# Performance work log

Measured on AMD Instinct MI355X. Metric: run time of the kernel, lower is better.

The kernel has to match this reference:

```python
import jax, jax.numpy as jnp
import numpy as np


def setup_inputs() -> dict:
    key = jax.random.key(0)
    ks = jax.random.split(key, 8)
    C, mid, H, W, N = 256, 32, 64, 64, 4
    x = jax.random.normal(ks[0], (N, C, H, W), dtype=jnp.float32)
    # 1x1 conv weights squeezed to [out_ch, in_ch]; small init scale like kaiming
    s = 1.0 / np.sqrt(C)
    Wq = jax.random.normal(ks[1], (mid, C), dtype=jnp.float32) * s
    bq = jnp.zeros((mid,), dtype=jnp.float32)
    Wk = jax.random.normal(ks[2], (mid, C), dtype=jnp.float32) * s
    bk = jnp.zeros((mid,), dtype=jnp.float32)
    Wv = jax.random.normal(ks[3], (C, C), dtype=jnp.float32) * s
    bv = jnp.zeros((C,), dtype=jnp.float32)
    gamma = jax.random.uniform(ks[4], (1,), dtype=jnp.float32)
    return {"x": x, "Wq": Wq, "bq": bq, "Wk": Wk, "bk": bk, "Wv": Wv, "bv": bv, "gamma": gamma}


def reference(x, Wq, bq, Wk, bk, Wv, bv, gamma):
    N, C, H, W = x.shape
    xf = x.reshape(N, C, H * W)  # [N, C, S]
    # 1x1 convs are channel-mixing GEMMs
    Q = jnp.einsum('mc,ncs->nms', Wq, xf) + bq[:, None]  # [N, mid, S]
    K = jnp.einsum('mc,ncs->nms', Wk, xf) + bk[:, None]  # [N, mid, S]
    V = jnp.einsum('dc,ncs->nds', Wv, xf) + bv[:, None]  # [N, C, S]
    # A[s, t] = softmax_t( Q[:, s] . K[:, t] )
    scores = jnp.einsum('nms,nmt->nst', Q, K)            # [N, S, S]
    A = jax.nn.softmax(scores, axis=-1)
    # out = V @ A^T : out[:, s] = sum_t A[s, t] * V[:, t]
    out = jnp.einsum('ndt,nst->nds', V, A).reshape(N, C, H, W)
    return x + gamma[0] * out
```

## Files before the change

### kernel.cpp

```cpp
#include <hip/hip_runtime.h>
#include <hip/hip_bf16.h>
#include <stdint.h>

#define S_LEN 4096
#define LOG2E 1.44269504088896f
#define SMAX  40.0f

typedef __attribute__((ext_vector_type(8)))  short short8;
typedef __attribute__((ext_vector_type(8)))  _Float16 half8;
typedef __attribute__((ext_vector_type(4)))  float f32x4;
typedef __attribute__((ext_vector_type(16))) float f32x16;
typedef __attribute__((ext_vector_type(2)))  unsigned int u32x2;
typedef __attribute__((ext_vector_type(4)))  unsigned int u32x4;

#define OFF_V     ((size_t)0)
#define OFF_QT    (OFF_V + (size_t)(8u<<20))
#define OFF_KT    (OFF_QT + (size_t)(1u<<20))
#define OFF_WVBF  (OFF_KT + (size_t)(1u<<20))
#define OFF_WQH   (OFF_WVBF + (size_t)(128*1024))
#define OFF_WQL   (OFF_WQH + (size_t)(16*1024))
#define OFF_WKH   (OFF_WQL + (size_t)(16*1024))
#define OFF_WKL   (OFF_WKH + (size_t)(16*1024))

__device__ __forceinline__ unsigned short f2bf(float f) {
    __hip_bfloat16 h = __float2bfloat16(f);
    return *(unsigned short*)&h;
}
__device__ __forceinline__ float bf2f(unsigned short u) {
    return __bfloat162float(*(__hip_bfloat16*)&u);
}
__device__ __forceinline__ unsigned pk2(float a, float b) {
    return (unsigned)f2bf(a) | ((unsigned)f2bf(b) << 16);
}
__device__ __forceinline__ unsigned short f2h(float f) {
    _Float16 h = (_Float16)f;
    return *(unsigned short*)&h;
}
union S8U { u32x4 u; short8 s; };
union H8U { short8 s; half8 h; };

__device__ __forceinline__ void gl_lds16(const void* g, void* l) {
    __builtin_amdgcn_global_load_lds(
        (const __attribute__((address_space(1))) unsigned int*)g,
        (__attribute__((address_space(3))) unsigned int*)(unsigned int)(size_t)l,
        16, 0, 0);
}

#define Z16 {0.f,0.f,0.f,0.f,0.f,0.f,0.f,0.f,0.f,0.f,0.f,0.f,0.f,0.f,0.f,0.f}
#define MFMA32  __builtin_amdgcn_mfma_f32_32x32x16_bf16
#define MFMA32H __builtin_amdgcn_mfma_f32_32x32x16_f16

__global__ __launch_bounds__(256) void wprep(const float* __restrict__ Wq,
                                             const float* __restrict__ Wk,
                                             const float* __restrict__ Wv,
                                             unsigned short* __restrict__ wvbf,
                                             unsigned short* __restrict__ wqh,
                                             unsigned short* __restrict__ wql,
                                             unsigned short* __restrict__ wkh,
                                             unsigned short* __restrict__ wkl)
{
    const int b = blockIdx.x;
    if (b < 64) {
        int i = b * 1024 + threadIdx.x * 4;
        f32x4 w = *(const f32x4*)(Wv + i);
        u32x2 pk;
        pk[0] = pk2(w[0], w[1]);
        pk[1] = pk2(w[2], w[3]);
        *(u32x2*)(wvbf + i) = pk;
    } else {
        const float* Wsrc = (b == 64) ? Wq : Wk;
        float scale = (b == 64) ? LOG2E : 1.f;
        unsigned short* oh = (b == 64) ? wqh : wkh;
        unsigned short* ol = (b == 64) ? wql : wkl;
        int t = threadIdx.x;
#pragma unroll
        for (int ii = 0; ii < 4; ii++) {
            int ent = t * 4 + ii;
            int m = ent & 31, hh = (ent >> 5) & 1, kc = ent >> 6;
#pragma unroll
            for (int e = 0; e < 8; e++) {
                int c = kc * 16 + hh * 8 + e;
                float wv = Wsrc[m * 256 + c] * scale;
                unsigned short wh = f2bf(wv);
                oh[ent * 8 + e] = wh;
                ol[ent * 8 + e] = f2bf(wv - bf2f(wh));
            }
        }
    }
}

__global__ __launch_bounds__(256) void qkv_fused(
    const float* __restrict__ x,
    const unsigned short* __restrict__ wqh, const unsigned short* __restrict__ wql,
    const unsigned short* __restrict__ wkh, const unsigned short* __restrict__ wkl,
    const unsigned short* __restrict__ wvbf,
    const float* __restrict__ bq, const float* __restrict__ bk, const float* __restrict__ bv,
    unsigned short* __restrict__ qt, unsigned short* __restrict__ kt,
    unsigned char* __restrict__ Vsw)
{
    const int tid = threadIdx.x;
    const int bidx = blockIdx.x;
    const int n = bidx >> 7, t0 = (bidx & 127) * 32;
    const int w = tid >> 6, l = tid & 63;
    const int l31 = l & 31, h = l >> 5;

    __shared__ float xs[256 * 36];

    {
        const int c0 = tid >> 3;
        const int tq = (tid & 7) * 4;
        const float* xp = x + ((size_t)n * 256 + c0) * S_LEN + t0 + tq;
#pragma unroll
        for (int p = 0; p < 8; p++) {
            f32x4 v = *(const f32x4*)(xp + (size_t)p * 32 * S_LEN);
            *(f32x4*)(&xs[(c0 + p * 32) * 36 + tq]) = v;
        }
    }
    __syncthreads();

    if (w < 2) {
        const unsigned short* WH = w ? wkh : wqh;
        const unsigned short* WL = w ? wkl : wql;
        f32x16 a = Z16;
#pragma unroll
        for (int kc = 0; kc < 16; kc++) {
            short8 ah, al;
#pragma unroll
            for (int e = 0; e < 8; e++) {
                float f = xs[(kc * 16 + h * 8 + e) * 36 + l31];
                unsigned short hb = f2bf(f);
                ah[e] = (short)hb;
                al[e] = (short)f2bf(f - bf2f(hb));
            }
            const short8 bh = *(const short8*)(WH + ((kc * 2 + h) * 32 + l31) * 8);
            const short8 bl = *(const short8*)(WL + ((kc * 2 + h) * 32 + l31) * 8);
            a = MFMA32(ah, bh, a, 0, 0, 0);
            a = MFMA32(al, bh, a, 0, 0, 0);
            a = MFMA32(ah, bl, a, 0, 0, 0);
        }
        float bias = w ? bk[l31] : bq[l31] * LOG2E;
        unsigned short* oh = w ? kt : qt;
#pragma unroll
        for (int r = 0; r < 16; r++) {
            int trow = (r & 3) + 8 * (r >> 2) + 4 * h;
            size_t o = ((size_t)n * S_LEN + t0 + trow) * 32 + l31;
            oh[o] = f2h(a[r] + bias);
        }
    } else {
        const int dh = w - 2;
        f32x16 acc[4];
#pragma unroll
        for (int dt = 0; dt < 4; dt++) acc[dt] = (f32x16)Z16;
#pragma unroll
        for (int kc = 0; kc < 16; kc++) {
            short8 ah;
#pragma unroll
            for (int e = 0; e < 8; e++)
                ah[e] = (short)f2bf(xs[(kc * 16 + h * 8 + e) * 36 + l31]);
#pragma unroll
            for (int dt = 0; dt < 4; dt++) {
                const short8 b = *(const short8*)(wvbf +
                    (size_t)(dh * 128 + dt * 32 + l31) * 256 + kc * 16 + h * 8);
                acc[dt] = MFMA32(ah, b, acc[dt], 0, 0, 0);
            }
        }
        unsigned char* img = Vsw + ((size_t)(n * 128) + (t0 >> 5)) * 16384;
#pragma unroll
        for (int dt = 0; dt < 4; dt++) {
            int d = dh * 128 + dt * 32 + l31;
            float bvv = bv[d];
#pragma unroll
            for (int g = 0; g < 4; g++) {
                u32x2 pkv;
                pkv[0] = pk2(acc[dt][4*g+0] + bvv, acc[dt][4*g+1] + bvv);
                pkv[1] = pk2(acc[dt][4*g+2] + bvv, acc[dt][4*g+3] + bvv);
                *(u32x2*)(img + (g >> 1) * 8192 + d * 32 + h * 16 + (g & 1) * 8) = pkv;
            }
        }
    }
}

__global__ __launch_bounds__(512, 2) void attn(
    const unsigned short* __restrict__ qt, const unsigned short* __restrict__ kt,
    const unsigned char* __restrict__ Vsw, const float* __restrict__ x,
    const float* __restrict__ gamma, float* __restrict__ out)
{
    const int bid = blockIdx.x;
    const int n = bid & 3;
    const int S0 = (bid >> 2) * 64;
    const int tid = threadIdx.x;
    const int w = tid >> 6, l = tid & 63;
    const int i = w & 1, q = w >> 1;
    const int l31 = l & 31, h = l >> 5;

    __shared__ __align__(16) unsigned char smem[131072 + 1024];
    float* mldsp = (float*)(smem + 131072);

    const size_t qb = ((size_t)n * S_LEN + S0 + i * 32 + l31) * 32 + 8 * h;
    H8U q0, q1;
    q0.s = *(const short8*)(qt + qb);
    q1.s = *(const short8*)(qt + qb + 16);

    f32x16 acc[8];
#pragma unroll
    for (int dt = 0; dt < 8; dt++) acc[dt] = (f32x16)Z16;
    float l_run = 0.f;

    const unsigned short* Kt = kt + (size_t)n * S_LEN * 32;
    const unsigned char* Vimg = Vsw + ((size_t)n * 128 + (size_t)q * 32) * 16384 + i * 8192;
    unsigned char* bufA = smem + (q * 2) * 16384;

    {
        const unsigned char* sp = Vimg + l * 16;
#pragma unroll
        for (int k = 0; k < 8; k++)
            gl_lds16(sp + k * 1024, bufA + i * 8192 + k * 1024);
    }
    size_t kb = (size_t)(q * 1024 + l31) * 32 + 8 * h;
    H8U k0, k1;
    k0.s = *(const short8*)(Kt + kb);
    k1.s = *(const short8*)(Kt + kb + 16);
    short8 paA = {0,0,0,0,0,0,0,0}, paB = {0,0,0,0,0,0,0,0};
    __syncthreads();

    const int vread = l31 * 32 + h * 16;

    for (int j = 0; j < 32; ++j) {
        __builtin_amdgcn_s_setprio(1);
        f32x16 sD = Z16;
        sD = MFMA32H(k0.h, q0.h, sD, 0, 0, 0);
        sD = MFMA32H(k1.h, q1.h, sD, 0, 0, 0);
        __builtin_amdgcn_s_setprio(0);

        if (j < 31) {
            kb += 1024;
            k0.s = *(const short8*)(Kt + kb);
            k1.s = *(const short8*)(Kt + kb + 16);
        }

        if (j > 0) {
            const unsigned char* rb = bufA + (1 - (j & 1)) * 16384;
            __builtin_amdgcn_s_setprio(1);
#pragma unroll
            for (int dt = 0; dt < 8; dt++) {
                const unsigned char* vrow = rb + dt * 1024 + vread;
                short8 v0 = *(const short8*)(vrow);
                short8 v1 = *(const short8*)(vrow + 8192);
                acc[dt] = MFMA32(v0, paA, acc[dt], 0, 0, 0);
                acc[dt] = MFMA32(v1, paB, acc[dt], 0, 0, 0);
            }
            __builtin_amdgcn_s_setprio(0);
        }

        float pe[16];
#pragma unroll
        for (int r = 0; r < 16; r++) pe[r] = __builtin_amdgcn_exp2f(sD[r] - SMAX);
        float ls = ((pe[0] + pe[1]) + (pe[2] + pe[3])) + ((pe[4] + pe[5]) + (pe[6] + pe[7]))
                 + ((pe[8] + pe[9]) + (pe[10] + pe[11])) + ((pe[12] + pe[13]) + (pe[14] + pe[15]));
        l_run += ls;

        unsigned pb[8];
#pragma unroll
        for (int i2 = 0; i2 < 8; i2++) pb[i2] = pk2(pe[2 * i2], pe[2 * i2 + 1]);
        S8U ca, cb;
        ca.u = (u32x4){pb[0], pb[1], pb[2], pb[3]};
        cb.u = (u32x4){pb[4], pb[5], pb[6], pb[7]};
        paA = ca.s;
        paB = cb.s;

        __syncthreads();

        if (j < 31) {
            const unsigned char* sp = Vimg + (size_t)(j + 1) * 16384 + l * 16;
            unsigned char* wb = bufA + ((j + 1) & 1) * 16384;
#pragma unroll
            for (int k = 0; k < 8; k++)
                gl_lds16(sp + k * 1024, wb + i * 8192 + k * 1024);
        }
    }

    {
        const unsigned char* rb = bufA + 16384;
        __builtin_amdgcn_s_setprio(1);
#pragma unroll
        for (int dt = 0; dt < 8; dt++) {
            const unsigned char* vrow = rb + dt * 1024 + vread;
            short8 v0 = *(const short8*)(vrow);
            short8 v1 = *(const short8*)(vrow + 8192);
            acc[dt] = MFMA32(v0, paA, acc[dt], 0, 0, 0);
            acc[dt] = MFMA32(v1, paB, acc[dt], 0, 0, 0);
        }
        __builtin_amdgcn_s_setprio(0);
    }

    l_run += __shfl_xor(l_run, 32);
    if (h == 0) mldsp[(q * 2 + i) * 32 + l31] = l_run;
    __syncthreads();

    float rden = 1.f / (mldsp[(0 * 2 + i) * 32 + l31] + mldsp[(1 * 2 + i) * 32 + l31]
                      + mldsp[(2 * 2 + i) * 32 + l31] + mldsp[(3 * 2 + i) * 32 + l31]);
    const float g = gamma[0];
    const int s = S0 + i * 32 + l31;

#pragma unroll
    for (int rb2 = 0; rb2 < 2; rb2++) {
        __syncthreads();
        unsigned char* myreg = smem + q * 32768 + i * 16384;
#pragma unroll
        for (int dtl = 0; dtl < 4; dtl++) {
            int dt = rb2 * 4 + dtl;
#pragma unroll
            for (int qd = 0; qd < 4; qd++) {
                f32x4 v = { acc[dt][4*qd], acc[dt][4*qd+1],
                            acc[dt][4*qd+2], acc[dt][4*qd+3] };
                *(f32x4*)(myreg + dtl * 4096 + qd * 1024 + l * 16) = v;
            }
        }
        __syncthreads();
        const int dtc = rb2 * 4 + q;
#pragma unroll
        for (int qd = 0; qd < 4; qd++) {
            f32x4 vs = {0.f, 0.f, 0.f, 0.f};
#pragma unroll
            for (int qq = 0; qq < 4; qq++) {
                f32x4 v = *(const f32x4*)(smem + qq * 32768 + i * 16384
                                          + q * 4096 + qd * 1024 + l * 16);
                vs[0] += v[0]; vs[1] += v[1]; vs[2] += v[2]; vs[3] += v[3];
            }
#pragma unroll
            for (int j = 0; j < 4; j++) {
                int d = dtc * 32 + j + 8 * qd + 4 * h;
                size_t idx = ((size_t)n * 256 + d) * S_LEN + s;
                out[idx] = x[idx] + g * vs[j] * rden;
            }
        }
    }
}

extern "C" void kernel_launch(void* const* d_in, const int* in_sizes, int n_in,
                              void* d_out, int out_size, void* d_ws, size_t ws_size,
                              hipStream_t stream) {
    const float* x     = (const float*)d_in[0];
    const float* Wq    = (const float*)d_in[1];
    const float* bq    = (const float*)d_in[2];
    const float* Wk    = (const float*)d_in[3];
    const float* bk    = (const float*)d_in[4];
    const float* Wv    = (const float*)d_in[5];
    const float* bv    = (const float*)d_in[6];
    const float* gamma = (const float*)d_in[7];
    float* out = (float*)d_out;

    unsigned char* ws = (unsigned char*)d_ws;
    unsigned char*  Vsw  = ws + OFF_V;
    unsigned short* qt   = (unsigned short*)(ws + OFF_QT);
    unsigned short* kt   = (unsigned short*)(ws + OFF_KT);
    unsigned short* wvbf = (unsigned short*)(ws + OFF_WVBF);
    unsigned short* wqh  = (unsigned short*)(ws + OFF_WQH);
    unsigned short* wql  = (unsigned short*)(ws + OFF_WQL);
    unsigned short* wkh  = (unsigned short*)(ws + OFF_WKH);
    unsigned short* wkl  = (unsigned short*)(ws + OFF_WKL);

    wprep<<<dim3(66), dim3(256), 0, stream>>>(Wq, Wk, Wv, wvbf, wqh, wql, wkh, wkl);
    qkv_fused<<<dim3(512), dim3(256), 0, stream>>>(x, wqh, wql, wkh, wkl, wvbf,
                                                   bq, bk, bv, qt, kt, Vsw);
    attn<<<dim3(256), dim3(512), 0, stream>>>(qt, kt, Vsw, x, gamma, out);
}
```

Measured before the change: 82.49 us.

## Stage V projection writes through LDS and stagger exp/MFMA phases across waves

In the projection kernel, the V tile is first written into shared memory in its swizzled layout, then copied to global memory with coalesced 16-byte stores by all threads. Matching barriers are added to the Q/K branch. In the attention loop, half the waves run the PV MFMAs before the exp/softmax work and the other half run exp first. This lets MFMA and transcendental work from different waves overlap, and the setprio around the QK MFMAs is removed. The cost is extra barriers and an LDS round trip in the projection kernel, plus some code duplication.

After: 98.97 us. +20.0%, slower.

```diff
diff --git a/kernel.cpp b/kernel.cpp
--- a/kernel.cpp
+++ b/kernel.cpp
@@ -146,6 +146,8 @@
             size_t o = ((size_t)n * S_LEN + t0 + trow) * 32 + l31;
             oh[o] = f2h(a[r] + bias);
         }
+        __syncthreads();
+        __syncthreads();
     } else {
         const int dh = w - 2;
         f32x16 acc[4];
@@ -164,7 +166,8 @@
                 acc[dt] = MFMA32(ah, b, acc[dt], 0, 0, 0);
             }
         }
-        unsigned char* img = Vsw + ((size_t)(n * 128) + (t0 >> 5)) * 16384;
+        __syncthreads();
+        unsigned char* vimg = (unsigned char*)xs;
 #pragma unroll
         for (int dt = 0; dt < 4; dt++) {
             int d = dh * 128 + dt * 32 + l31;
@@ -174,9 +177,19 @@
                 u32x2 pkv;
                 pkv[0] = pk2(acc[dt][4*g+0] + bvv, acc[dt][4*g+1] + bvv);
                 pkv[1] = pk2(acc[dt][4*g+2] + bvv, acc[dt][4*g+3] + bvv);
-                *(u32x2*)(img + (g >> 1) * 8192 + d * 32 + h * 16 + (g & 1) * 8) = pkv;
-            }
-        }
+                *(u32x2*)(vimg + (g >> 1) * 8192 + d * 32 + h * 16 + (g & 1) * 8) = pkv;
+            }
+        }
+        __syncthreads();
+    }
+
+    {
+        unsigned char* img = Vsw + ((size_t)(n * 128) + (t0 >> 5)) * 16384;
+        const unsigned char* vimg = (const unsigned char*)xs;
+#pragma unroll
+        for (int c2 = 0; c2 < 4; c2++)
+            *(u32x4*)(img + c2 * 4096 + tid * 16) =
+                *(const u32x4*)(vimg + c2 * 4096 + tid * 16);
     }
 }
 
@@ -191,6 +204,7 @@
     const int tid = threadIdx.x;
     const int w = tid >> 6, l = tid & 63;
     const int i = w & 1, q = w >> 1;
+    const int ph = (w >> 2) & 1;
     const int l31 = l & 31, h = l >> 5;
 
     __shared__ __align__(16) unsigned char smem[131072 + 1024];
@@ -226,11 +240,9 @@
     const int vread = l31 * 32 + h * 16;
 
     for (int j = 0; j < 32; ++j) {
-        __builtin_amdgcn_s_setprio(1);
         f32x16 sD = Z16;
         sD = MFMA32H(k0.h, q0.h, sD, 0, 0, 0);
         sD = MFMA32H(k1.h, q1.h, sD, 0, 0, 0);
-        __builtin_amdgcn_s_setprio(0);
 
         if (j < 31) {
             kb += 1024;
@@ -238,35 +250,63 @@
             k1.s = *(const short8*)(Kt + kb + 16);
         }
 
-        if (j > 0) {
-            const unsigned char* rb = bufA + (1 - (j & 1)) * 16384;
-            __builtin_amdgcn_s_setprio(1);
-#pragma unroll
-            for (int dt = 0; dt < 8; dt++) {
-                const unsigned char* vrow = rb + dt * 1024 + vread;
-                short8 v0 = *(const short8*)(vrow);
-                short8 v1 = *(const short8*)(vrow + 8192);
-                acc[dt] = MFMA32(v0, paA, acc[dt], 0, 0, 0);
-                acc[dt] = MFMA32(v1, paB, acc[dt], 0, 0, 0);
-            }
-            __builtin_amdgcn_s_setprio(0);
-        }
-
-        float pe[16];
-#pragma unroll
-        for (int r = 0; r < 16; r++) pe[r] = __builtin_amdgcn_exp2f(sD[r] - SMAX);
-        float ls = ((pe[0] + pe[1]) + (pe[2] + pe[3])) + ((pe[4] + pe[5]) + (pe[6] + pe[7]))
-                 + ((pe[8] + pe[9]) + (pe[10] + pe[11])) + ((pe[12] + pe[13]) + (pe[14] + pe[15]));
-        l_run += ls;
-
-        unsigned pb[8];
-#pragma unroll
-        for (int i2 = 0; i2 < 8; i2++) pb[i2] = pk2(pe[2 * i2], pe[2 * i2 + 1]);
-        S8U ca, cb;
-        ca.u = (u32x4){pb[0], pb[1], pb[2], pb[3]};
-        cb.u = (u32x4){pb[4], pb[5], pb[6], pb[7]};
-        paA = ca.s;
-        paB = cb.s;
+        const unsigned char* rb = bufA + (1 - (j & 1)) * 16384;
+
+        if (ph == 0) {
+            if (j > 0) {
+                __builtin_amdgcn_s_setprio(1);
+#pragma unroll
+                for (int dt = 0; dt < 8; dt++) {
+                    const unsigned char* vrow = rb + dt * 1024 + vread;
+                    short8 v0 = *(const short8*)(vrow);
+                    short8 v1 = *(const short8*)(vrow + 8192);
+                    acc[dt] = MFMA32(v0, paA, acc[dt], 0, 0, 0);
+                    acc[dt] = MFMA32(v1, paB, acc[dt], 0, 0, 0);
+                }
+                __builtin_amdgcn_s_setprio(0);
+            }
+            float pe[16];
+#pragma unroll
+            for (int r = 0; r < 16; r++) pe[r] = __builtin_amdgcn_exp2f(sD[r] - SMAX);
+            float ls = ((pe[0]+pe[1])+(pe[2]+pe[3])) + ((pe[4]+pe[5])+(pe[6]+pe[7]))
+                     + ((pe[8]+pe[9])+(pe[10]+pe[11])) + ((pe[12]+pe[13])+(pe[14]+pe[15]));
+            l_run += ls;
+            unsigned pb[8];
+#pragma unroll
+            for (int i2 = 0; i2 < 8; i2++) pb[i2] = pk2(pe[2*i2], pe[2*i2+1]);
+            S8U ca, cb;
+            ca.u = (u32x4){pb[0], pb[1], pb[2], pb[3]};
+            cb.u = (u32x4){pb[4], pb[5], pb[6], pb[7]};
+            paA = ca.s;
+            paB = cb.s;
+        } else {
+            float pe[16];
+#pragma unroll
+            for (int r = 0; r < 16; r++) pe[r] = __builtin_amdgcn_exp2f(sD[r] - SMAX);
+            float ls = ((pe[0]+pe[1])+(pe[2]+pe[3])) + ((pe[4]+pe[5])+(pe[6]+pe[7]))
+                     + ((pe[8]+pe[9])+(pe[10]+pe[11])) + ((pe[12]+pe[13])+(pe[14]+pe[15]));
+            l_run += ls;
+            if (j > 0) {
+                __builtin_amdgcn_s_setprio(1);
+#pragma unroll
+                for (int dt = 0; dt < 8; dt++) {
+                    const unsigned char* vrow = rb + dt * 1024 + vread;
+                    short8 v0 = *(const short8*)(vrow);
+                    short8 v1 = *(const short8*)(vrow + 8192);
+                    acc[dt] = MFMA32(v0, paA, acc[dt], 0, 0, 0);
+                    acc[dt] = MFMA32(v1, paB, acc[dt], 0, 0, 0);
+                }
+                __builtin_amdgcn_s_setprio(0);
+            }
+            unsigned pb[8];
+#pragma unroll
+            for (int i2 = 0; i2 < 8; i2++) pb[i2] = pk2(pe[2*i2], pe[2*i2+1]);
+            S8U ca, cb;
+            ca.u = (u32x4){pb[0], pb[1], pb[2], pb[3]};
+            cb.u = (u32x4){pb[4], pb[5], pb[6], pb[7]};
+            paA = ca.s;
+            paB = cb.s;
+        }
 
         __syncthreads();
 
```
